# Optimization experiments

Measured on AMD Instinct MI355X. Metric: run time of the kernel, lower is better.

The kernel has to match this reference:

```python
import jax, jax.numpy as jnp
import numpy as np

N_POINTS = 131072
N_ANCHORS = 2048


def setup_inputs() -> dict:
    key = jax.random.key(0)
    k1, k2, k3, k4 = jax.random.split(key, 4)
    locations3d = jax.random.normal(k1, (N_POINTS, 3), dtype=jnp.float32)
    anchor_locations3d = jax.random.normal(k2, (N_ANCHORS, 3), dtype=jnp.float32)
    anchor_coeffs = jax.random.normal(k3, (N_ANCHORS,), dtype=jnp.float32)
    # per-anchor widths, kept strictly positive in [0.1, 1.0)
    anchor_parameters = jax.random.uniform(k4, (N_ANCHORS,), dtype=jnp.float32) * 0.9 + 0.1
    return {
        "locations3d": locations3d,
        "anchor_locations3d": anchor_locations3d,
        "anchor_coeffs": anchor_coeffs,
        "anchor_parameters": anchor_parameters,
    }


def potential_operator(locations3d, anchor_locations3d, anchor_parameters):
    # Pairwise squared distances via the expanded form (avoids [N,M,3] intermediate):
    x_sq = jnp.sum(locations3d * locations3d, axis=-1, keepdims=True)          # [N,1]
    a_sq = jnp.sum(anchor_locations3d * anchor_locations3d, axis=-1)            # [M]
    cross = locations3d @ anchor_locations3d.T                                  # [N,M]
    sqdist = x_sq + a_sq[None, :] - 2.0 * cross
    sqdist = jnp.maximum(sqdist, 0.0)
    inv_two_w2 = 0.5 / (anchor_parameters * anchor_parameters)                  # [M]
    return jnp.exp(-sqdist * inv_two_w2[None, :])                               # [N,M]


def reference(locations3d, anchor_locations3d, anchor_coeffs, anchor_parameters):
    K = potential_operator(locations3d, anchor_locations3d, anchor_parameters)  # [N,M]
    return K @ anchor_coeffs                                                    # [N]
```

## Files before the change

### kernel.cpp

```cpp
#include <hip/hip_runtime.h>

#define N_POINTS  131072
#define N_ANCHORS 2048
#define CHUNKS    16
#define M_PER     (N_ANCHORS / CHUNKS)
#define THREADS   256
#define PTS       4
#define PT_STRIDE (N_POINTS / PTS)
#define LOG2E     1.4426950408889634f

typedef float v2f __attribute__((ext_vector_type(2)));

__global__ __launch_bounds__(256, 8) void linear_potential_main(
    const float* __restrict__ xloc,
    const float* __restrict__ aloc,
    const float* __restrict__ coeffs,
    const float* __restrict__ params,
    float* __restrict__ out)
{
    __shared__ float4 sA[M_PER];
    __shared__ float2 sB[M_PER];

    const int t     = threadIdx.x;
    const int mbase = blockIdx.y * M_PER;

    if (t < M_PER) {
        const int m  = mbase + t;
        const float a0 = aloc[3 * m + 0];
        const float a1 = aloc[3 * m + 1];
        const float a2 = aloc[3 * m + 2];
        const float w  = params[m];
        const float sp = -(0.5f * LOG2E) / (w * w);
        sA[t] = make_float4(-2.0f * sp * a0, -2.0f * sp * a1, -2.0f * sp * a2,
                            sp * (a0 * a0 + a1 * a1 + a2 * a2));
        sB[t] = make_float2(sp, coeffs[m]);
    }
    __syncthreads();

    const int tid = blockIdx.x * THREADS + t;
    const int n0 = tid;
    const int n1 = tid + PT_STRIDE;
    const int n2 = tid + 2 * PT_STRIDE;
    const int n3 = tid + 3 * PT_STRIDE;

    const v2f xa = { xloc[3 * n0 + 0], xloc[3 * n1 + 0] };
    const v2f ya = { xloc[3 * n0 + 1], xloc[3 * n1 + 1] };
    const v2f za = { xloc[3 * n0 + 2], xloc[3 * n1 + 2] };
    const v2f xb = { xloc[3 * n2 + 0], xloc[3 * n3 + 0] };
    const v2f yb = { xloc[3 * n2 + 1], xloc[3 * n3 + 1] };
    const v2f zb = { xloc[3 * n2 + 2], xloc[3 * n3 + 2] };

    const v2f ssa = __builtin_elementwise_fma(xa, xa,
                    __builtin_elementwise_fma(ya, ya, za * za));
    const v2f ssb = __builtin_elementwise_fma(xb, xb,
                    __builtin_elementwise_fma(yb, yb, zb * zb));

    v2f acca = { 0.0f, 0.0f };
    v2f accb = { 0.0f, 0.0f };

    #pragma unroll 8
    for (int mm = 0; mm < M_PER; ++mm) {
        const float4 p = sA[mm];
        const float2 c = sB[mm];
        const v2f pw = { p.w, p.w };
        const v2f px = { p.x, p.x };
        const v2f py = { p.y, p.y };
        const v2f pz = { p.z, p.z };
        const v2f sp = { c.x, c.x };
        const v2f cf = { c.y, c.y };

        v2f arga = __builtin_elementwise_fma(px, xa,
                   __builtin_elementwise_fma(py, ya,
                   __builtin_elementwise_fma(pz, za,
                   __builtin_elementwise_fma(sp, ssa, pw))));
        v2f argb = __builtin_elementwise_fma(px, xb,
                   __builtin_elementwise_fma(py, yb,
                   __builtin_elementwise_fma(pz, zb,
                   __builtin_elementwise_fma(sp, ssb, pw))));

        v2f ea = { __builtin_amdgcn_exp2f(arga.x), __builtin_amdgcn_exp2f(arga.y) };
        v2f eb = { __builtin_amdgcn_exp2f(argb.x), __builtin_amdgcn_exp2f(argb.y) };

        acca = __builtin_elementwise_fma(cf, ea, acca);
        accb = __builtin_elementwise_fma(cf, eb, accb);
    }

    atomicAdd(&out[n0], acca.x);
    atomicAdd(&out[n1], acca.y);
    atomicAdd(&out[n2], accb.x);
    atomicAdd(&out[n3], accb.y);
}

extern "C" void kernel_launch(void* const* d_in, const int* in_sizes, int n_in,
                              void* d_out, int out_size, void* d_ws, size_t ws_size,
                              hipStream_t stream) {
    const float* xloc   = (const float*)d_in[0];
    const float* aloc   = (const float*)d_in[1];
    const float* coeffs = (const float*)d_in[2];
    const float* params = (const float*)d_in[3];
    float* out = (float*)d_out;

    hipMemsetAsync(d_out, 0, N_POINTS * sizeof(float), stream);

    linear_potential_main<<<dim3(N_POINTS / (THREADS * PTS), CHUNKS),
                            dim3(THREADS), 0, stream>>>(
        xloc, aloc, coeffs, params, out);
}
```

Measured before the change: 99.51 us.

## Precompute anchor params in separate kernel and read via uniform global loads

```diff
diff --git a/kernel.cpp b/kernel.cpp
--- a/kernel.cpp
+++ b/kernel.cpp
@@ -11,32 +11,41 @@
 
 typedef float v2f __attribute__((ext_vector_type(2)));
 
+struct __align__(64) Anchor {
+    v2f r0, r1, r2, q, sp, cf;
+    v2f pad0, pad1;
+};
+
+__global__ void precompute_anchors(const float* __restrict__ aloc,
+                                   const float* __restrict__ coeffs,
+                                   const float* __restrict__ params,
+                                   Anchor* __restrict__ A) {
+    int m = blockIdx.x * blockDim.x + threadIdx.x;
+    if (m >= N_ANCHORS) return;
+    const float a0 = aloc[3 * m + 0];
+    const float a1 = aloc[3 * m + 1];
+    const float a2 = aloc[3 * m + 2];
+    const float w  = params[m];
+    const float sp = -(0.5f * LOG2E) / (w * w);
+    const float r0 = -2.0f * sp * a0;
+    const float r1 = -2.0f * sp * a1;
+    const float r2 = -2.0f * sp * a2;
+    const float q  = sp * (a0 * a0 + a1 * a1 + a2 * a2);
+    const float cf = coeffs[m];
+    Anchor out;
+    out.r0 = (v2f){r0, r0};  out.r1 = (v2f){r1, r1};
+    out.r2 = (v2f){r2, r2};  out.q  = (v2f){q, q};
+    out.sp = (v2f){sp, sp};  out.cf = (v2f){cf, cf};
+    out.pad0 = (v2f){0.f, 0.f}; out.pad1 = (v2f){0.f, 0.f};
+    A[m] = out;
+}
+
 __global__ __launch_bounds__(256, 8) void linear_potential_main(
     const float* __restrict__ xloc,
-    const float* __restrict__ aloc,
-    const float* __restrict__ coeffs,
-    const float* __restrict__ params,
+    const Anchor* __restrict__ anchors,
     float* __restrict__ out)
 {
-    __shared__ float4 sA[M_PER];
-    __shared__ float2 sB[M_PER];
-
-    const int t     = threadIdx.x;
-    const int mbase = blockIdx.y * M_PER;
-
-    if (t < M_PER) {
-        const int m  = mbase + t;
-        const float a0 = aloc[3 * m + 0];
-        const float a1 = aloc[3 * m + 1];
-        const float a2 = aloc[3 * m + 2];
-        const float w  = params[m];
-        const float sp = -(0.5f * LOG2E) / (w * w);
-        sA[t] = make_float4(-2.0f * sp * a0, -2.0f * sp * a1, -2.0f * sp * a2,
-                            sp * (a0 * a0 + a1 * a1 + a2 * a2));
-        sB[t] = make_float2(sp, coeffs[m]);
-    }
-    __syncthreads();
-
+    const int t   = threadIdx.x;
     const int tid = blockIdx.x * THREADS + t;
     const int n0 = tid;
     const int n1 = tid + PT_STRIDE;
@@ -58,25 +67,26 @@
     v2f acca = { 0.0f, 0.0f };
     v2f accb = { 0.0f, 0.0f };
 
-    #pragma unroll 8
+    const Anchor* __restrict__ ach = anchors + blockIdx.y * M_PER;
+
+    #pragma unroll 4
     for (int mm = 0; mm < M_PER; ++mm) {
-        const float4 p = sA[mm];
-        const float2 c = sB[mm];
-        const v2f pw = { p.w, p.w };
-        const v2f px = { p.x, p.x };
-        const v2f py = { p.y, p.y };
-        const v2f pz = { p.z, p.z };
-        const v2f sp = { c.x, c.x };
-        const v2f cf = { c.y, c.y };
+        const v2f r0 = ach[mm].r0;
+        const v2f r1 = ach[mm].r1;
+        const v2f r2 = ach[mm].r2;
+        const v2f q  = ach[mm].q;
+        const v2f sp = ach[mm].sp;
+        const v2f cf = ach[mm].cf;
 
-        v2f arga = __builtin_elementwise_fma(px, xa,
-                   __builtin_elementwise_fma(py, ya,
-                   __builtin_elementwise_fma(pz, za,
-                   __builtin_elementwise_fma(sp, ssa, pw))));
-        v2f argb = __builtin_elementwise_fma(px, xb,
-                   __builtin_elementwise_fma(py, yb,
-                   __builtin_elementwise_fma(pz, zb,
-                   __builtin_elementwise_fma(sp, ssb, pw))));
+        v2f arga = __builtin_elementwise_fma(sp, ssa, q);
+        arga     = __builtin_elementwise_fma(r0, xa, arga);
+        arga     = __builtin_elementwise_fma(r1, ya, arga);
+        arga     = __builtin_elementwise_fma(r2, za, arga);
+
+        v2f argb = __builtin_elementwise_fma(sp, ssb, q);
+        argb     = __builtin_elementwise_fma(r0, xb, argb);
+        argb     = __builtin_elementwise_fma(r1, yb, argb);
+        argb     = __builtin_elementwise_fma(r2, zb, argb);
 
         v2f ea = { __builtin_amdgcn_exp2f(arga.x), __builtin_amdgcn_exp2f(arga.y) };
         v2f eb = { __builtin_amdgcn_exp2f(argb.x), __builtin_amdgcn_exp2f(argb.y) };
@@ -100,9 +110,14 @@
     const float* params = (const float*)d_in[3];
     float* out = (float*)d_out;
 
+    Anchor* A = (Anchor*)d_ws;
+
     hipMemsetAsync(d_out, 0, N_POINTS * sizeof(float), stream);
+
+    precompute_anchors<<<dim3(N_ANCHORS / 256), dim3(256), 0, stream>>>(
+        aloc, coeffs, params, A);
 
     linear_potential_main<<<dim3(N_POINTS / (THREADS * PTS), CHUNKS),
                             dim3(THREADS), 0, stream>>>(
-        xloc, aloc, coeffs, params, out);
+        xloc, A, out);
 }
```

After: 102.9 us. 1.03x slower.
